# Kernel tuning notes

Measured on AMD Instinct MI355X. Metric: run time of the kernel, lower is better.

## Reference

```python
import jax, jax.numpy as jnp
import numpy as np

B, S, E, F = 8, 2048, 1024, 4096
EPS = 1e-5


def _layer_norm(x, gamma, beta):
    mu = jnp.mean(x, axis=-1, keepdims=True)
    var = jnp.mean((x - mu) ** 2, axis=-1, keepdims=True)
    return (x - mu) * jax.lax.rsqrt(var + EPS) * gamma + beta


def setup_inputs() -> dict:
    key = jax.random.key(0)
    ks = jax.random.split(key, 16)
    s = 0.02
    return {
        "x": jax.random.normal(ks[0], (B, S, E), dtype=jnp.float32),
        "Wq": jax.random.normal(ks[1], (E, E), dtype=jnp.float32) * s,
        "bq": jnp.zeros((E,), dtype=jnp.float32),
        "Wk": jax.random.normal(ks[2], (E, E), dtype=jnp.float32) * s,
        "bk": jnp.zeros((E,), dtype=jnp.float32),
        "Wv": jax.random.normal(ks[3], (E, E), dtype=jnp.float32) * s,
        "bv": jnp.zeros((E,), dtype=jnp.float32),
        "gamma1": jnp.ones((E,), dtype=jnp.float32),
        "beta1": jnp.zeros((E,), dtype=jnp.float32),
        "W1": jax.random.normal(ks[4], (E, F), dtype=jnp.float32) * s,
        "b1": jnp.zeros((F,), dtype=jnp.float32),
        "W2": jax.random.normal(ks[5], (F, E), dtype=jnp.float32) * s,
        "b2": jnp.zeros((E,), dtype=jnp.float32),
        "gamma2": jnp.ones((E,), dtype=jnp.float32),
        "beta2": jnp.zeros((E,), dtype=jnp.float32),
    }


def reference(x, Wq, bq, Wk, bk, Wv, bv, gamma1, beta1, W1, b1, W2, b2, gamma2, beta2):
    # Single-head attention exactly as the torch forward (neurogenesis=False path).
    q = x @ Wq + bq  # [B,S,E]
    k = x @ Wk + bk
    v = x @ Wv + bv
    scores = jnp.einsum('bse,bte->bst', q, k) / jnp.sqrt(jnp.float32(E))
    attn = jax.nn.softmax(scores, axis=-1)
    attn_out = jnp.einsum('bst,bte->bse', attn, v)
    # dropout is identity in eval mode
    h = _layer_norm(x + attn_out, gamma1, beta1)
    ffn = jax.nn.relu(h @ W1 + b1) @ W2 + b2
    out = _layer_norm(h + ffn, gamma2, beta2)
    return (out, k, q, v)
```

## Files before the change

kernel.cpp:

```cpp
#include <hip/hip_runtime.h>
#include <hip/hip_bf16.h>
#include <stdint.h>

typedef __attribute__((ext_vector_type(8))) short s16x8;
typedef __attribute__((ext_vector_type(4))) float f32x4;

static constexpr int Bb = 8, Ss = 2048, Ee = 1024, Ff = 4096;
static constexpr int M_TOK = Bb * Ss;
static constexpr size_t OUT_SLOT = (size_t)M_TOK * Ee;

__device__ inline unsigned short f2bf(float f) {
  unsigned int u = __float_as_uint(f);
  unsigned int r = (u + 0x7FFFu + ((u >> 16) & 1u)) >> 16;
  return (unsigned short)r;
}
__device__ inline float bf2f(unsigned short h) {
  return __uint_as_float(((unsigned int)h) << 16);
}

__device__ inline void gload16(const unsigned short* g, const unsigned short* l) {
  __builtin_amdgcn_global_load_lds(
      (const __attribute__((address_space(1))) void*)g,
      (__attribute__((address_space(3))) void*)(unsigned short*)l, 16, 0, 0);
}

__global__ __launch_bounds__(256) void k_cvt_f32_bf16(const float* __restrict__ in,
                                                      unsigned short* __restrict__ out, int n4) {
  int i = blockIdx.x * blockDim.x + threadIdx.x;
  int stride = gridDim.x * blockDim.x;
  for (; i < n4; i += stride) {
    float4 v = ((const float4*)in)[i];
    ushort4 o;
    o.x = f2bf(v.x); o.y = f2bf(v.y); o.z = f2bf(v.z); o.w = f2bf(v.w);
    ((ushort4*)out)[i] = o;
  }
}

__global__ __launch_bounds__(256) void k_concat3(const float* __restrict__ a,
                                                 const float* __restrict__ b,
                                                 const float* __restrict__ c,
                                                 float* __restrict__ out) {
  int i = blockIdx.x * 256 + threadIdx.x;
  const float* src = (i < 1024) ? a : (i < 2048) ? b : c;
  out[i] = src[i & 1023];
}

__global__ __launch_bounds__(256) void k_transpose_w(const float* __restrict__ in,
                                                     unsigned short* __restrict__ out,
                                                     int R, int C) {
  __shared__ float t[32][33];
  int c0 = blockIdx.x * 32, r0 = blockIdx.y * 32;
  int tx = threadIdx.x, ty = threadIdx.y;
  for (int i = ty; i < 32; i += 8)
    t[i][tx] = in[(size_t)(r0 + i) * C + c0 + tx];
  __syncthreads();
  for (int i = ty; i < 32; i += 8)
    out[(size_t)(c0 + i) * R + r0 + tx] = f2bf(t[tx][i]);
}

__global__ __launch_bounds__(256) void k_transpose_v(const unsigned short* __restrict__ v,
                                                     unsigned short* __restrict__ vT) {
  __shared__ unsigned short t[32][33];
  int b = blockIdx.z;
  const unsigned short* in = v + (size_t)b * Ss * Ee;
  unsigned short* out = vT + (size_t)b * Ee * Ss;
  int c0 = blockIdx.x * 32, r0 = blockIdx.y * 32;
  int tx = threadIdx.x, ty = threadIdx.y;
  for (int i = ty; i < 32; i += 8)
    t[i][tx] = in[(size_t)(r0 + i) * Ee + c0 + tx];
  __syncthreads();
  for (int i = ty; i < 32; i += 8)
    out[(size_t)(c0 + i) * Ss + r0 + tx] = t[tx][i];
}

template <bool QKV, bool WF32, bool WB16, bool RELU, bool HAS_BIAS>
__global__ __launch_bounds__(512, 2) void k_gemm256(const unsigned short* __restrict__ A,
                                                    const unsigned short* __restrict__ Bt,
                                                    float* __restrict__ Cf,
                                                    unsigned short* __restrict__ Cb,
                                                    const float* __restrict__ bias,
                                                    int M, int N, int K,
                                                    long aBatch, long bBatch, long cBatch,
                                                    float scale) {
  __shared__ unsigned short lds[4][2][256 * 32];
  const int tid = threadIdx.x;
  const int lane = tid & 63;
  const int wid = tid >> 6;
  const int wr = wid >> 2, wc = wid & 3;

  const int gx = gridDim.x, gy = gridDim.y;
  const int nwg = gx * gy;
  const int id = blockIdx.y * gx + blockIdx.x;
  const int qq = nwg >> 3;
  const int s = (id & 7) * qq + (id >> 3);
  const int g4 = s / (gy * 4);
  const int r4 = s - g4 * gy * 4;
  const int m0 = (g4 * 4 + (r4 & 3)) * 256;
  const int n0 = (r4 >> 2) * 256;
  const int z = blockIdx.z;
  A += (size_t)z * aBatch;
  Bt += (size_t)z * bBatch;

  const int srow = tid >> 2;
  const int csrc = (tid & 3) ^ ((tid >> 3) & 3);
  const unsigned short* ga0 = A + (size_t)(m0 + srow) * K + csrc * 8;
  const unsigned short* ga1 = A + (size_t)(m0 + 128 + srow) * K + csrc * 8;
  const unsigned short* gb0 = Bt + (size_t)(n0 + srow) * K + csrc * 8;
  const unsigned short* gb1 = Bt + (size_t)(n0 + 128 + srow) * K + csrc * 8;
  const int waveDst = (wid << 9);

  auto STAGE_A = [&](int step) {
    const int slot = step & 3;
    const size_t ko = (size_t)step << 5;
    const unsigned short* la = &lds[slot][0][0];
    gload16(ga0 + ko, la + waveDst);
    gload16(ga1 + ko, la + 4096 + waveDst);
  };
  auto STAGE_B = [&](int step) {
    const int slot = step & 3;
    const size_t ko = (size_t)step << 5;
    const unsigned short* lb = &lds[slot][1][0];
    gload16(gb0 + ko, lb + waveDst);
    gload16(gb1 + ko, lb + 4096 + waveDst);
  };

  f32x4 acc[8][4] = {};
  const int fr = lane & 15;
  const int cc = ((lane >> 4) ^ ((fr >> 1) & 3)) * 8;
  const int nt = K >> 5;

  STAGE_A(0); STAGE_B(0); STAGE_A(1); STAGE_B(1); STAGE_A(2); STAGE_B(2);
  asm volatile("s_waitcnt vmcnt(8)" ::: "memory");
  __builtin_amdgcn_s_barrier();
  asm volatile("" ::: "memory");

  for (int t = 0; t < nt; ++t) {
    const int slot = t & 3;
    const unsigned short* la = &lds[slot][0][0];
    const unsigned short* lb = &lds[slot][1][0];
    s16x8 ra[4], rb[4], ra2[4];
#pragma unroll
    for (int ni = 0; ni < 4; ++ni)
      rb[ni] = *(const s16x8*)(lb + ((wc * 64 + ni * 16 + fr) * 32 + cc));
#pragma unroll
    for (int mi = 0; mi < 4; ++mi)
      ra[mi] = *(const s16x8*)(la + ((wr * 128 + mi * 16 + fr) * 32 + cc));
    if (t + 3 < nt) {
      STAGE_A(t + 3);
      asm volatile("s_waitcnt vmcnt(6)" ::: "memory");
    } else if (t + 2 < nt) {
      asm volatile("s_waitcnt vmcnt(4)" ::: "memory");
    } else {
      asm volatile("s_waitcnt vmcnt(0)" ::: "memory");
    }
    __builtin_amdgcn_s_barrier();
    asm volatile("" ::: "memory");
    __builtin_amdgcn_s_setprio(1);
#pragma unroll
    for (int mi = 0; mi < 4; ++mi)
#pragma unroll
      for (int ni = 0; ni < 4; ++ni)
        acc[mi][ni] = __builtin_amdgcn_mfma_f32_16x16x32_bf16(ra[mi], rb[ni], acc[mi][ni], 0, 0, 0);
#pragma unroll
    for (int mi = 0; mi < 4; ++mi)
      ra2[mi] = *(const s16x8*)(la + ((wr * 128 + (mi + 4) * 16 + fr) * 32 + cc));
    if (t + 3 < nt) STAGE_B(t + 3);
    __builtin_amdgcn_s_setprio(0);
    __builtin_amdgcn_s_barrier();
    asm volatile("" ::: "memory");
    __builtin_amdgcn_s_setprio(1);
#pragma unroll
    for (int mi = 0; mi < 4; ++mi)
#pragma unroll
      for (int ni = 0; ni < 4; ++ni)
        acc[mi + 4][ni] = __builtin_amdgcn_mfma_f32_16x16x32_bf16(ra2[mi], rb[ni], acc[mi + 4][ni], 0, 0, 0);
    __builtin_amdgcn_s_setprio(0);
  }

  const int er = lane & 15, eq = lane >> 4;
#pragma unroll
  for (int mi = 0; mi < 8; ++mi) {
#pragma unroll
    for (int ni = 0; ni < 4; ++ni) {
#pragma unroll
      for (int r = 0; r < 4; ++r) {
        int row = m0 + wr * 128 + mi * 16 + eq * 4 + r;
        int col = n0 + wc * 64 + ni * 16 + er;
        float v = acc[mi][ni][r] * scale;
        if (HAS_BIAS) v += bias[col];
        if (RELU) v = v > 0.f ? v : 0.f;
        if (QKV) {
          int which = col >> 10;
          int c2 = col & 1023;
          size_t ro = (size_t)row * 1024 + c2;
          int fslot = (which == 0) ? 2 : (which == 1) ? 1 : 3;
          __builtin_nontemporal_store(v, &Cf[(size_t)fslot * OUT_SLOT + ro]);
          Cb[(size_t)which * OUT_SLOT + ro] = f2bf(v);
        } else {
          size_t idx = (size_t)z * cBatch + (size_t)row * N + col;
          if (WF32) Cf[idx] = v;
          if (WB16) Cb[idx] = f2bf(v);
        }
      }
    }
  }
}

__global__ __launch_bounds__(256) void k_softmax(unsigned short* __restrict__ sa) {
  __shared__ float red[4];
  const int row = blockIdx.x;
  const int tid = threadIdx.x;
  unsigned short* sr = sa + (size_t)row * Ss;
  ushort4 u0 = ((const ushort4*)sr)[tid];
  ushort4 u1 = ((const ushort4*)sr)[tid + 256];
  float e[8];
  e[0] = bf2f(u0.x); e[1] = bf2f(u0.y); e[2] = bf2f(u0.z); e[3] = bf2f(u0.w);
  e[4] = bf2f(u1.x); e[5] = bf2f(u1.y); e[6] = bf2f(u1.z); e[7] = bf2f(u1.w);
  float m = fmaxf(fmaxf(fmaxf(e[0], e[1]), fmaxf(e[2], e[3])),
                  fmaxf(fmaxf(e[4], e[5]), fmaxf(e[6], e[7])));
  for (int s = 1; s < 64; s <<= 1) m = fmaxf(m, __shfl_xor(m, s, 64));
  if ((tid & 63) == 0) red[tid >> 6] = m;
  __syncthreads();
  m = fmaxf(fmaxf(red[0], red[1]), fmaxf(red[2], red[3]));
  __syncthreads();
  float sum = 0.f;
#pragma unroll
  for (int j = 0; j < 8; ++j) { e[j] = __expf(e[j] - m); sum += e[j]; }
  for (int s = 1; s < 64; s <<= 1) sum += __shfl_xor(sum, s, 64);
  if ((tid & 63) == 0) red[tid >> 6] = sum;
  __syncthreads();
  sum = red[0] + red[1] + red[2] + red[3];
  float inv = 1.f / sum;
  ushort4 o0, o1;
  o0.x = f2bf(e[0] * inv); o0.y = f2bf(e[1] * inv);
  o0.z = f2bf(e[2] * inv); o0.w = f2bf(e[3] * inv);
  o1.x = f2bf(e[4] * inv); o1.y = f2bf(e[5] * inv);
  o1.z = f2bf(e[6] * inv); o1.w = f2bf(e[7] * inv);
  ((ushort4*)sr)[tid] = o0;
  ((ushort4*)sr)[tid + 256] = o1;
}

template <bool A_F32, bool OUT_F32>
__global__ __launch_bounds__(256) void k_ln(const void* __restrict__ a,
                                            const unsigned short* __restrict__ bb,
                                            const float* __restrict__ gamma,
                                            const float* __restrict__ beta,
                                            void* __restrict__ outp) {
  __shared__ float red[4];
  const int row = blockIdx.x;
  const int tid = threadIdx.x;
  float v[4];
  if (A_F32) {
    float4 av = ((const float4*)((const float*)a + (size_t)row * Ee))[tid];
    v[0] = av.x; v[1] = av.y; v[2] = av.z; v[3] = av.w;
  } else {
    ushort4 av = ((const ushort4*)((const unsigned short*)a + (size_t)row * Ee))[tid];
    v[0] = bf2f(av.x); v[1] = bf2f(av.y); v[2] = bf2f(av.z); v[3] = bf2f(av.w);
  }
  ushort4 bv = ((const ushort4*)(bb + (size_t)row * Ee))[tid];
  v[0] += bf2f(bv.x); v[1] += bf2f(bv.y); v[2] += bf2f(bv.z); v[3] += bf2f(bv.w);
  float s = v[0] + v[1] + v[2] + v[3];
  float q = v[0] * v[0] + v[1] * v[1] + v[2] * v[2] + v[3] * v[3];
  for (int sh = 1; sh < 64; sh <<= 1) {
    s += __shfl_xor(s, sh, 64);
    q += __shfl_xor(q, sh, 64);
  }
  if ((tid & 63) == 0) red[tid >> 6] = s;
  __syncthreads();
  s = red[0] + red[1] + red[2] + red[3];
  __syncthreads();
  if ((tid & 63) == 0) red[tid >> 6] = q;
  __syncthreads();
  q = red[0] + red[1] + red[2] + red[3];
  float mu = s * (1.f / Ee);
  float var = q * (1.f / Ee) - mu * mu;
  float rinv = rsqrtf(var + 1e-5f);
  int c = tid * 4;
  float o0 = (v[0] - mu) * rinv * gamma[c + 0] + beta[c + 0];
  float o1 = (v[1] - mu) * rinv * gamma[c + 1] + beta[c + 1];
  float o2 = (v[2] - mu) * rinv * gamma[c + 2] + beta[c + 2];
  float o3 = (v[3] - mu) * rinv * gamma[c + 3] + beta[c + 3];
  if (OUT_F32) {
    f32x4 o = {o0, o1, o2, o3};
    __builtin_nontemporal_store(o, (f32x4*)((float*)outp + (size_t)row * Ee) + tid);
  } else {
    ushort4 o;
    o.x = f2bf(o0); o.y = f2bf(o1); o.z = f2bf(o2); o.w = f2bf(o3);
    ((ushort4*)((unsigned short*)outp + (size_t)row * Ee))[tid] = o;
  }
}

extern "C" void kernel_launch(void* const* d_in, const int* in_sizes, int n_in,
                              void* d_out, int out_size, void* d_ws, size_t ws_size,
                              hipStream_t stream) {
  const float* x = (const float*)d_in[0];
  const float* Wq = (const float*)d_in[1];
  const float* bq = (const float*)d_in[2];
  const float* Wk = (const float*)d_in[3];
  const float* bk = (const float*)d_in[4];
  const float* Wv = (const float*)d_in[5];
  const float* bv = (const float*)d_in[6];
  const float* g1 = (const float*)d_in[7];
  const float* be1 = (const float*)d_in[8];
  const float* W1 = (const float*)d_in[9];
  const float* b1 = (const float*)d_in[10];
  const float* W2 = (const float*)d_in[11];
  const float* b2 = (const float*)d_in[12];
  const float* g2 = (const float*)d_in[13];
  const float* be2 = (const float*)d_in[14];

  float* out = (float*)d_out;

  char* ws = (char*)d_ws;
  unsigned short* xb    = (unsigned short*)(ws + 0);
  unsigned short* WqkvT = (unsigned short*)(ws + 33554432ull);
  unsigned short* W1T   = (unsigned short*)(ws + 39845888ull);
  unsigned short* W2T   = (unsigned short*)(ws + 48234496ull);
  unsigned short* qb    = (unsigned short*)(ws + 56623104ull);
  unsigned short* kb    = (unsigned short*)(ws + 90177536ull);
  unsigned short* vb    = (unsigned short*)(ws + 123731968ull);
  unsigned short* scb   = (unsigned short*)(ws + 157286400ull);
  unsigned short* vT    = (unsigned short*)(ws + 224395264ull);
  float*          bqkv  = (float*)(ws + 257949696ull);
  unsigned short* ao    = (unsigned short*)(ws + 56623104ull);
  unsigned short* hb    = (unsigned short*)(ws + 90177536ull);
  unsigned short* f1b   = (unsigned short*)(ws + 157286400ull);
  unsigned short* f2b   = (unsigned short*)(ws + 123731968ull);

  dim3 tb(32, 8);
  k_cvt_f32_bf16<<<2048, 256, 0, stream>>>(x, xb, M_TOK * Ee / 4);
  k_transpose_w<<<dim3(32, 32), tb, 0, stream>>>(Wq, WqkvT, Ee, Ee);
  k_transpose_w<<<dim3(32, 32), tb, 0, stream>>>(Wk, WqkvT + 1048576, Ee, Ee);
  k_transpose_w<<<dim3(32, 32), tb, 0, stream>>>(Wv, WqkvT + 2097152, Ee, Ee);
  k_transpose_w<<<dim3(128, 32), tb, 0, stream>>>(W1, W1T, Ee, Ff);
  k_transpose_w<<<dim3(32, 128), tb, 0, stream>>>(W2, W2T, Ff, Ee);
  k_concat3<<<12, 256, 0, stream>>>(bq, bk, bv, bqkv);
  k_gemm256<true, true, true, false, true><<<dim3(64, 12, 1), 512, 0, stream>>>(
      xb, WqkvT, out, qb, bqkv, M_TOK, 3072, Ee, 0, 0, 0, 1.f);
  k_gemm256<false, false, true, false, false><<<dim3(8, 8, 8), 512, 0, stream>>>(
      qb, kb, nullptr, scb, nullptr, Ss, Ss, Ee, (long)Ss * Ee, (long)Ss * Ee, (long)Ss * Ss,
      0.03125f);
  k_softmax<<<Bb * Ss, 256, 0, stream>>>(scb);
  k_transpose_v<<<dim3(32, 64, 8), tb, 0, stream>>>(vb, vT);
  k_gemm256<false, false, true, false, false><<<dim3(8, 4, 8), 512, 0, stream>>>(
      scb, vT, nullptr, ao, nullptr, Ss, Ee, Ss, (long)Ss * Ss, (long)Ee * Ss, (long)Ss * Ee, 1.f);
  k_ln<false, false><<<M_TOK, 256, 0, stream>>>(xb, ao, g1, be1, hb);
  k_gemm256<false, false, true, true, true><<<dim3(64, 16, 1), 512, 0, stream>>>(
      hb, W1T, nullptr, f1b, b1, M_TOK, Ff, Ee, 0, 0, 0, 1.f);
  k_gemm256<false, false, true, false, true><<<dim3(64, 4, 1), 512, 0, stream>>>(
      f1b, W2T, nullptr, f2b, b2, M_TOK, Ee, Ff, 0, 0, 0, 1.f);
  k_ln<false, true><<<M_TOK, 256, 0, stream>>>(hb, f2b, g2, be2, out);
}
```

Before: 644.5 us.

## Fuse softmax into QK/PV GEMMs via partial stats and write V transposed

```diff
diff --git a/kernel.cpp b/kernel.cpp
--- a/kernel.cpp
+++ b/kernel.cpp
@@ -58,22 +58,22 @@
     out[(size_t)(c0 + i) * R + r0 + tx] = f2bf(t[tx][i]);
 }
 
-__global__ __launch_bounds__(256) void k_transpose_v(const unsigned short* __restrict__ v,
-                                                     unsigned short* __restrict__ vT) {
-  __shared__ unsigned short t[32][33];
-  int b = blockIdx.z;
-  const unsigned short* in = v + (size_t)b * Ss * Ee;
-  unsigned short* out = vT + (size_t)b * Ee * Ss;
-  int c0 = blockIdx.x * 32, r0 = blockIdx.y * 32;
-  int tx = threadIdx.x, ty = threadIdx.y;
-  for (int i = ty; i < 32; i += 8)
-    t[i][tx] = in[(size_t)(r0 + i) * Ee + c0 + tx];
-  __syncthreads();
-  for (int i = ty; i < 32; i += 8)
-    out[(size_t)(c0 + i) * Ss + r0 + tx] = t[tx][i];
-}
-
-template <bool QKV, bool WF32, bool WB16, bool RELU, bool HAS_BIAS>
+__global__ __launch_bounds__(256) void k_smcombine(const float* __restrict__ partials,
+                                                   float* __restrict__ stats) {
+  int i = blockIdx.x * 256 + threadIdx.x;
+  int z = i >> 11, row = i & 2047;
+  float m = -3.0e38f, s = 0.f;
+#pragma unroll
+  for (int j = 0; j < 32; ++j) {
+    float2 p = ((const float2*)partials)[((size_t)z * 32 + j) * 2048 + row];
+    float nm = fmaxf(m, p.x);
+    s = s * __expf(m - nm) + p.y * __expf(p.x - nm);
+    m = nm;
+  }
+  ((float2*)stats)[i] = make_float2(m, 1.f / s);
+}
+
+template <bool QKV, bool SSTAT, bool SMAX, bool WF32, bool WB16, bool RELU, bool HAS_BIAS>
 __global__ __launch_bounds__(512, 2) void k_gemm256(const unsigned short* __restrict__ A,
                                                     const unsigned short* __restrict__ Bt,
                                                     float* __restrict__ Cf,
@@ -81,7 +81,10 @@
                                                     const float* __restrict__ bias,
                                                     int M, int N, int K,
                                                     long aBatch, long bBatch, long cBatch,
-                                                    float scale) {
+                                                    float scale,
+                                                    float* __restrict__ partials,
+                                                    const float* __restrict__ stats,
+                                                    unsigned short* __restrict__ Vt) {
   __shared__ unsigned short lds[4][2][256 * 32];
   const int tid = threadIdx.x;
   const int lane = tid & 63;
@@ -108,6 +111,12 @@
   const unsigned short* gb0 = Bt + (size_t)(n0 + srow) * K + csrc * 8;
   const unsigned short* gb1 = Bt + (size_t)(n0 + 128 + srow) * K + csrc * 8;
   const int waveDst = (wid << 9);
+
+  float2 st0 = make_float2(0.f, 0.f), st1 = make_float2(0.f, 0.f);
+  if (SMAX) {
+    st0 = ((const float2*)stats)[(size_t)z * 2048 + m0 + srow];
+    st1 = ((const float2*)stats)[(size_t)z * 2048 + m0 + 128 + srow];
+  }
 
   auto STAGE_A = [&](int step) {
     const int slot = step & 3;
@@ -123,18 +132,44 @@
     gload16(gb0 + ko, lb + waveDst);
     gload16(gb1 + ko, lb + 4096 + waveDst);
   };
+  auto EXPWRITE = [&](int step, s16x8 c0, s16x8 c1) {
+    const int slot = step & 3;
+    unsigned short* la = (unsigned short*)&lds[slot][0][0];
+    s16x8 o0, o1;
+#pragma unroll
+    for (int j = 0; j < 8; ++j) {
+      o0[j] = (short)f2bf(__expf(bf2f((unsigned short)c0[j]) - st0.x) * st0.y);
+      o1[j] = (short)f2bf(__expf(bf2f((unsigned short)c1[j]) - st1.x) * st1.y);
+    }
+    *(s16x8*)(la + waveDst + lane * 8) = o0;
+    *(s16x8*)(la + 4096 + waveDst + lane * 8) = o1;
+  };
 
   f32x4 acc[8][4] = {};
   const int fr = lane & 15;
   const int cc = ((lane >> 4) ^ ((fr >> 1) & 3)) * 8;
   const int nt = K >> 5;
 
-  STAGE_A(0); STAGE_B(0); STAGE_A(1); STAGE_B(1); STAGE_A(2); STAGE_B(2);
-  asm volatile("s_waitcnt vmcnt(8)" ::: "memory");
+  s16x8 rA0, rA1, rB0, rB1;
+
+  if (!SMAX) {
+    STAGE_A(0); STAGE_B(0); STAGE_A(1); STAGE_B(1); STAGE_A(2); STAGE_B(2);
+    asm volatile("s_waitcnt vmcnt(8)" ::: "memory");
+  } else {
+    s16x8 p00 = *(const s16x8*)(ga0 + 0),  p01 = *(const s16x8*)(ga1 + 0);
+    s16x8 p10 = *(const s16x8*)(ga0 + 32), p11 = *(const s16x8*)(ga1 + 32);
+    s16x8 p20 = *(const s16x8*)(ga0 + 64), p21 = *(const s16x8*)(ga1 + 64);
+    rA0 = *(const s16x8*)(ga0 + 96); rA1 = *(const s16x8*)(ga1 + 96);
+    STAGE_B(0); STAGE_B(1); STAGE_B(2);
+    EXPWRITE(0, p00, p01);
+    EXPWRITE(1, p10, p11);
+    EXPWRITE(2, p20, p21);
+    asm volatile("s_waitcnt vmcnt(4)" ::: "memory");
+  }
   __builtin_amdgcn_s_barrier();
   asm volatile("" ::: "memory");
 
-  for (int t = 0; t < nt; ++t) {
+  auto TILE = [&](int t, s16x8& cur0, s16x8& cur1, s16x8& nxt0, s16x8& nxt1) {
     const int slot = t & 3;
     const unsigned short* la = &lds[slot][0][0];
     const unsigned short* lb = &lds[slot][1][0];
@@ -145,13 +180,26 @@
 #pragma unroll
     for (int mi = 0; mi < 4; ++mi)
       ra[mi] = *(const s16x8*)(la + ((wr * 128 + mi * 16 + fr) * 32 + cc));
-    if (t + 3 < nt) {
-      STAGE_A(t + 3);
-      asm volatile("s_waitcnt vmcnt(6)" ::: "memory");
-    } else if (t + 2 < nt) {
-      asm volatile("s_waitcnt vmcnt(4)" ::: "memory");
+    if (SMAX) {
+      if (t + 4 < nt) {
+        nxt0 = *(const s16x8*)(ga0 + ((size_t)(t + 4) << 5));
+        nxt1 = *(const s16x8*)(ga1 + ((size_t)(t + 4) << 5));
+      }
+      if (t + 3 < nt) {
+        EXPWRITE(t + 3, cur0, cur1);
+        STAGE_B(t + 3);
+      } else {
+        asm volatile("s_waitcnt vmcnt(0)" ::: "memory");
+      }
     } else {
-      asm volatile("s_waitcnt vmcnt(0)" ::: "memory");
+      if (t + 3 < nt) {
+        STAGE_A(t + 3);
+        asm volatile("s_waitcnt vmcnt(6)" ::: "memory");
+      } else if (t + 2 < nt) {
+        asm volatile("s_waitcnt vmcnt(4)" ::: "memory");
+      } else {
+        asm volatile("s_waitcnt vmcnt(0)" ::: "memory");
+      }
     }
     __builtin_amdgcn_s_barrier();
     asm volatile("" ::: "memory");
@@ -164,7 +212,7 @@
 #pragma unroll
     for (int mi = 0; mi < 4; ++mi)
       ra2[mi] = *(const s16x8*)(la + ((wr * 128 + (mi + 4) * 16 + fr) * 32 + cc));
-    if (t + 3 < nt) STAGE_B(t + 3);
+    if (!SMAX && t + 3 < nt) STAGE_B(t + 3);
     __builtin_amdgcn_s_setprio(0);
     __builtin_amdgcn_s_barrier();
     asm volatile("" ::: "memory");
@@ -175,6 +223,11 @@
       for (int ni = 0; ni < 4; ++ni)
         acc[mi + 4][ni] = __builtin_amdgcn_mfma_f32_16x16x32_bf16(ra2[mi], rb[ni], acc[mi + 4][ni], 0, 0, 0);
     __builtin_amdgcn_s_setprio(0);
+  };
+
+  for (int t = 0; t < nt; t += 2) {
+    TILE(t, rA0, rA1, rB0, rB1);
+    TILE(t + 1, rB0, rB1, rA0, rA1);
   }
 
   const int er = lane & 15, eq = lane >> 4;
@@ -182,66 +235,74 @@
   for (int mi = 0; mi < 8; ++mi) {
 #pragma unroll
     for (int ni = 0; ni < 4; ++ni) {
+      const int rowb = m0 + wr * 128 + mi * 16 + eq * 4;
+      const int col = n0 + wc * 64 + ni * 16 + er;
+      float vv[4];
 #pragma unroll
       for (int r = 0; r < 4; ++r) {
-        int row = m0 + wr * 128 + mi * 16 + eq * 4 + r;
-        int col = n0 + wc * 64 + ni * 16 + er;
         float v = acc[mi][ni][r] * scale;
         if (HAS_BIAS) v += bias[col];
         if (RELU) v = v > 0.f ? v : 0.f;
-        if (QKV) {
-          int which = col >> 10;
-          int c2 = col & 1023;
-          size_t ro = (size_t)row * 1024 + c2;
-          int fslot = (which == 0) ? 2 : (which == 1) ? 1 : 3;
-          __builtin_nontemporal_store(v, &Cf[(size_t)fslot * OUT_SLOT + ro]);
-          Cb[(size_t)which * OUT_SLOT + ro] = f2bf(v);
+        vv[r] = v;
+      }
+      if (QKV) {
+        const int which = col >> 10;
+        const int c2 = col & 1023;
+        const int fslot = (which == 0) ? 2 : (which == 1) ? 1 : 3;
+#pragma unroll
+        for (int r = 0; r < 4; ++r)
+          __builtin_nontemporal_store(vv[r],
+              &Cf[(size_t)fslot * OUT_SLOT + (size_t)(rowb + r) * 1024 + c2]);
+        if (which == 2) {
+          const int zb = rowb >> 11, sX = rowb & 2047;
+          ushort4 o;
+          o.x = f2bf(vv[0]); o.y = f2bf(vv[1]); o.z = f2bf(vv[2]); o.w = f2bf(vv[3]);
+          *(ushort4*)(Vt + ((size_t)zb * Ee + c2) * Ss + sX) = o;
         } else {
-          size_t idx = (size_t)z * cBatch + (size_t)row * N + col;
-          if (WF32) Cf[idx] = v;
-          if (WB16) Cb[idx] = f2bf(v);
+#pragma unroll
+          for (int r = 0; r < 4; ++r)
+            Cb[(size_t)which * OUT_SLOT + (size_t)(rowb + r) * 1024 + c2] = f2bf(vv[r]);
         }
+      } else {
+#pragma unroll
+        for (int r = 0; r < 4; ++r) {
+          size_t idx = (size_t)z * cBatch + (size_t)(rowb + r) * N + col;
+          if (WF32) Cf[idx] = vv[r];
+          if (WB16) Cb[idx] = f2bf(vv[r]);
+        }
       }
     }
   }
-}
-
-__global__ __launch_bounds__(256) void k_softmax(unsigned short* __restrict__ sa) {
-  __shared__ float red[4];
-  const int row = blockIdx.x;
-  const int tid = threadIdx.x;
-  unsigned short* sr = sa + (size_t)row * Ss;
-  ushort4 u0 = ((const ushort4*)sr)[tid];
-  ushort4 u1 = ((const ushort4*)sr)[tid + 256];
-  float e[8];
-  e[0] = bf2f(u0.x); e[1] = bf2f(u0.y); e[2] = bf2f(u0.z); e[3] = bf2f(u0.w);
-  e[4] = bf2f(u1.x); e[5] = bf2f(u1.y); e[6] = bf2f(u1.z); e[7] = bf2f(u1.w);
-  float m = fmaxf(fmaxf(fmaxf(e[0], e[1]), fmaxf(e[2], e[3])),
-                  fmaxf(fmaxf(e[4], e[5]), fmaxf(e[6], e[7])));
-  for (int s = 1; s < 64; s <<= 1) m = fmaxf(m, __shfl_xor(m, s, 64));
-  if ((tid & 63) == 0) red[tid >> 6] = m;
-  __syncthreads();
-  m = fmaxf(fmaxf(red[0], red[1]), fmaxf(red[2], red[3]));
-  __syncthreads();
-  float sum = 0.f;
-#pragma unroll
-  for (int j = 0; j < 8; ++j) { e[j] = __expf(e[j] - m); sum += e[j]; }
-  for (int s = 1; s < 64; s <<= 1) sum += __shfl_xor(sum, s, 64);
-  if ((tid & 63) == 0) red[tid >> 6] = sum;
-  __syncthreads();
-  sum = red[0] + red[1] + red[2] + red[3];
-  float inv = 1.f / sum;
-  ushort4 o0, o1;
-  o0.x = f2bf(e[0] * inv); o0.y = f2bf(e[1] * inv);
-  o0.z = f2bf(e[2] * inv); o0.w = f2bf(e[3] * inv);
-  o1.x = f2bf(e[4] * inv); o1.y = f2bf(e[5] * inv);
-  o1.z = f2bf(e[6] * inv); o1.w = f2bf(e[7] * inv);
-  ((ushort4*)sr)[tid] = o0;
-  ((ushort4*)sr)[tid + 256] = o1;
-}
-
-template <bool A_F32, bool OUT_F32>
-__global__ __launch_bounds__(256) void k_ln(const void* __restrict__ a,
+
+  if (SSTAT) {
+#pragma unroll
+    for (int mi = 0; mi < 8; ++mi) {
+#pragma unroll
+      for (int r = 0; r < 4; ++r) {
+        float v0 = acc[mi][0][r] * scale, v1 = acc[mi][1][r] * scale;
+        float v2 = acc[mi][2][r] * scale, v3 = acc[mi][3][r] * scale;
+        float m = fmaxf(fmaxf(v0, v1), fmaxf(v2, v3));
+        float sm = __expf(v0 - m) + __expf(v1 - m) + __expf(v2 - m) + __expf(v3 - m);
+#pragma unroll
+        for (int d = 1; d < 16; d <<= 1) {
+          float om = __shfl_xor(m, d, 64);
+          float os = __shfl_xor(sm, d, 64);
+          float nm = fmaxf(m, om);
+          sm = sm * __expf(m - nm) + os * __expf(om - nm);
+          m = nm;
+        }
+        if ((lane & 15) == 0) {
+          int row = m0 + wr * 128 + mi * 16 + eq * 4 + r;
+          ((float2*)partials)[((size_t)(z * 8 + (n0 >> 8)) * 4 + wc) * 2048 + row] =
+              make_float2(m, sm);
+        }
+      }
+    }
+  }
+}
+
+template <bool OUT_F32>
+__global__ __launch_bounds__(256) void k_ln(const unsigned short* __restrict__ a,
                                             const unsigned short* __restrict__ bb,
                                             const float* __restrict__ gamma,
                                             const float* __restrict__ beta,
@@ -250,13 +311,8 @@
   const int row = blockIdx.x;
   const int tid = threadIdx.x;
   float v[4];
-  if (A_F32) {
-    float4 av = ((const float4*)((const float*)a + (size_t)row * Ee))[tid];
-    v[0] = av.x; v[1] = av.y; v[2] = av.z; v[3] = av.w;
-  } else {
-    ushort4 av = ((const ushort4*)((const unsigned short*)a + (size_t)row * Ee))[tid];
-    v[0] = bf2f(av.x); v[1] = bf2f(av.y); v[2] = bf2f(av.z); v[3] = bf2f(av.w);
-  }
+  ushort4 av = ((const ushort4*)(a + (size_t)row * Ee))[tid];
+  v[0] = bf2f(av.x); v[1] = bf2f(av.y); v[2] = bf2f(av.z); v[3] = bf2f(av.w);
   ushort4 bv = ((const ushort4*)(bb + (size_t)row * Ee))[tid];
   v[0] += bf2f(bv.x); v[1] += bf2f(bv.y); v[2] += bf2f(bv.z); v[3] += bf2f(bv.w);
   float s = v[0] + v[1] + v[2] + v[3];
@@ -318,7 +374,8 @@
   unsigned short* W2T   = (unsigned short*)(ws + 48234496ull);
   unsigned short* qb    = (unsigned short*)(ws + 56623104ull);
   unsigned short* kb    = (unsigned short*)(ws + 90177536ull);
-  unsigned short* vb    = (unsigned short*)(ws + 123731968ull);
+  float*          part  = (float*)(ws + 123731968ull);
+  float*          stats = (float*)(ws + 127926272ull);
   unsigned short* scb   = (unsigned short*)(ws + 157286400ull);
   unsigned short* vT    = (unsigned short*)(ws + 224395264ull);
   float*          bqkv  = (float*)(ws + 257949696ull);
@@ -335,19 +392,19 @@
   k_transpose_w<<<dim3(128, 32), tb, 0, stream>>>(W1, W1T, Ee, Ff);
   k_transpose_w<<<dim3(32, 128), tb, 0, stream>>>(W2, W2T, Ff, Ee);
   k_concat3<<<12, 256, 0, stream>>>(bq, bk, bv, bqkv);
-  k_gemm256<true, true, true, false, true><<<dim3(64, 12, 1), 512, 0, stream>>>(
-      xb, WqkvT, out, qb, bqkv, M_TOK, 3072, Ee, 0, 0, 0, 1.f);
-  k_gemm256<false, false, true, false, false><<<dim3(8, 8, 8), 512, 0, stream>>>(
+  k_gemm256<true, false, false, true, true, false, true><<<dim3(64, 12, 1), 512, 0, stream>>>(
+      xb, WqkvT, out, qb, bqkv, M_TOK, 3072, Ee, 0, 0, 0, 1.f, nullptr, nullptr, vT);
+  k_gemm256<false, true, false, false, true, false, false><<<dim3(8, 8, 8), 512, 0, stream>>>(
       qb, kb, nullptr, scb, nullptr, Ss, Ss, Ee, (long)Ss * Ee, (long)Ss * Ee, (long)Ss * Ss,
-      0.03125f);
-  k_softmax<<<Bb * Ss, 256, 0, stream>>>(scb);
-  k_transpose_v<<<dim3(32, 64, 8), tb, 0, stream>>>(vb, vT);
-  k_gemm256<false, false, true, false, false><<<dim3(8, 4, 8), 512, 0, stream>>>(
-      scb, vT, nullptr, ao, nullptr, Ss, Ee, Ss, (long)Ss * Ss, (long)Ee * Ss, (long)Ss * Ee, 1.f);
-  k_ln<false, false><<<M_TOK, 256, 0, stream>>>(xb, ao, g1, be1, hb);
-  k_gemm256<false, false, true, true, true><<<dim3(64, 16, 1), 512, 0, stream>>>(
-      hb, W1T, nullptr, f1b, b1, M_TOK, Ff, Ee, 0, 0, 0, 1.f);
-  k_gemm256<false, false, true, false, true><<<dim3(64, 4, 1), 512, 0, stream>>>(
-      f1b, W2T, nullptr, f2b, b2, M_TOK, Ee, Ff, 0, 0, 0, 1.f);
-  k_ln<false, true><<<M_TOK, 256, 0, stream>>>(hb, f2b, g2, be2, out);
-}
+      0.03125f, part, nullptr, nullptr);
+  k_smcombine<<<64, 256, 0, stream>>>(part, stats);
+  k_gemm256<false, false, true, false, true, false, false><<<dim3(8, 4, 8), 512, 0, stream>>>(
+      scb, vT, nullptr, ao, nullptr, Ss, Ee, Ss, (long)Ss * Ss, (long)Ee * Ss, (long)Ss * Ee,
+      1.f, nullptr, stats, nullptr);
+  k_ln<false><<<M_TOK, 256, 0, stream>>>(xb, ao, g1, be1, hb);
+  k_gemm256<false, false, false, false, true, true, true><<<dim3(64, 16, 1), 512, 0, stream>>>(
+      hb, W1T, nullptr, f1b, b1, M_TOK, Ff, Ee, 0, 0, 0, 1.f, nullptr, nullptr, nullptr);
+  k_gemm256<false, false, false, false, true, false, true><<<dim3(64, 4, 1), 512, 0, stream>>>(
+      f1b, W2T, nullptr, f2b, b2, M_TOK, Ee, Ff, 0, 0, 0, 1.f, nullptr, nullptr, nullptr);
+  k_ln<true><<<M_TOK, 256, 0, stream>>>(hb, f2b, g2, be2, out);
+}
```

Result: slower. 712.9 us (+10.6%).
